# Performance work log

Hardware: AMD Instinct MI355X
Metric: run time of the kernel (lower is better)

## Reference

```python
import jax, jax.numpy as jnp
import numpy as np
import math

# e3nn-style fully-connected Clebsch-Gordan tensor product
# irreps_in1 = 64x0e + 64x1e + 64x2e   (dim 576)
# irreps_in2 =  1x0e +  1x1e +  1x2e   (dim 9, e.g. spherical harmonics)
# irreps_out = 64x0e + 64x1e + 64x2e   (dim 576), shared weights
MUL1, MUL2, MULO = 64, 1, 64
LS = [0, 1, 2]
N_BATCH = 32768


def _su2_cg(j1, m1, j2, m2, j3, m3):
    # SU(2) Clebsch-Gordan coefficient <j1 m1 j2 m2 | j3 m3> (Racah formula)
    if m3 != m1 + m2:
        return 0.0
    f = math.factorial
    c = (2 * j3 + 1) * f(j1 + j2 - j3) * f(j1 - j2 + j3) * f(-j1 + j2 + j3) / f(j1 + j2 + j3 + 1)
    c = math.sqrt(c)
    c *= math.sqrt(f(j3 + m3) * f(j3 - m3) * f(j1 - m1) * f(j1 + m1) * f(j2 - m2) * f(j2 + m2))
    s = 0.0
    for k in range(max(0, j2 - j3 - m1, j1 - j3 + m2), min(j1 + j2 - j3, j1 - m1, j2 + m2) + 1):
        s += (-1.0) ** k / (f(k) * f(j1 + j2 - j3 - k) * f(j1 - m1 - k) * f(j2 + m2 - k)
                            * f(j3 - j2 + m1 + k) * f(j3 - j1 - m2 + k))
    return c * s


def _q_real_to_complex(l):
    # unitary change of basis, columns = real-SH index, rows = complex m (e3nn convention)
    q = np.zeros((2 * l + 1, 2 * l + 1), dtype=np.complex128)
    r2 = 1.0 / math.sqrt(2.0)
    for m in range(-l, 0):
        q[l + m, l + abs(m)] = r2
        q[l + m, l - abs(m)] = -1j * r2
    q[l, l] = 1.0
    for m in range(1, l + 1):
        q[l + m, l + m] = (-1) ** m * r2
        q[l + m, l - m] = 1j * (-1) ** m * r2
    return (-1j) ** l * q


def _real_cg(l1, l2, l3):
    # CG tensor in the real spherical-harmonic basis, unit Frobenius norm (wigner_3j-like)
    C = np.zeros((2 * l1 + 1, 2 * l2 + 1, 2 * l3 + 1), dtype=np.complex128)
    for m1 in range(-l1, l1 + 1):
        for m2 in range(-l2, l2 + 1):
            m3 = m1 + m2
            if abs(m3) <= l3:
                C[l1 + m1, l2 + m2, l3 + m3] = _su2_cg(l1, m1, l2, m2, l3, m3)
    U1, U2, U3 = _q_real_to_complex(l1), _q_real_to_complex(l2), _q_real_to_complex(l3)
    Cr = np.einsum('ia,jb,kc,ijk->abc', U1, U2, np.conj(U3), C)
    assert np.abs(Cr.imag).max() < 1e-9, 'real-basis CG should be real'
    Cr = Cr.real
    return (Cr / np.linalg.norm(Cr)).astype(np.float32)


PATHS = [(l1, l2, l3) for l1 in LS for l2 in LS for l3 in LS if abs(l1 - l2) <= l3 <= l1 + l2]
CG = {p: jnp.asarray(_real_cg(*p)) for p in PATHS}
N_PATHS_TO = {l3: sum(1 for p in PATHS if p[2] == l3) for l3 in LS}
ALPHA = {l3: 1.0 / math.sqrt(MUL1 * MUL2 * N_PATHS_TO[l3]) for l3 in LS}  # path normalization
WEIGHT_NUMEL = len(PATHS) * MUL1 * MUL2 * MULO  # 15 * 4096 = 61440
DIM1 = MUL1 * sum(2 * l + 1 for l in LS)  # 576
DIM2 = MUL2 * sum(2 * l + 1 for l in LS)  # 9


def _split1(x):
    segs, off = [], 0
    for l in LS:
        d = MUL1 * (2 * l + 1)
        segs.append(x[:, off:off + d].reshape(-1, MUL1, 2 * l + 1))
        off += d
    return segs


def _split2(y):
    segs, off = [], 0
    for l in LS:
        d = 2 * l + 1
        segs.append(y[:, off:off + d])
        off += d
    return segs


def tensor_product(x, y, W):
    # W (x (CG-otimes) y): per-path weighted Clebsch-Gordan contraction
    xs, ys = _split1(x), _split2(y)  # xs[l]: [N,64,2l+1], ys[l]: [N,2l+1]
    N = x.shape[0]
    outs = [jnp.zeros((N, MULO, 2 * l + 1), x.dtype) for l in LS]
    off = 0
    for (l1, l2, l3) in PATHS:
        Wp = W[off:off + MUL1 * MULO].reshape(MUL1, MULO)  # [u, w] (v = 1)
        off += MUL1 * MULO
        outs[l3] = outs[l3] + ALPHA[l3] * jnp.einsum(
            'nui,nj,ijk,uw->nwk', xs[l1], ys[l2], CG[(l1, l2, l3)], Wp)
    return jnp.concatenate([o.reshape(N, -1) for o in outs], axis=-1)  # [N, 576]


def setup_inputs() -> dict:
    key = jax.random.key(0)
    kx, ky, kw = jax.random.split(key, 3)
    x = jax.random.normal(kx, (N_BATCH, DIM1), dtype=jnp.float32)
    y = jax.random.normal(ky, (N_BATCH, DIM2), dtype=jnp.float32)
    W = jax.random.normal(kw, (WEIGHT_NUMEL,), dtype=jnp.float32)
    return {'x': x, 'y': y, 'W': W}


def reference(x, y, W):
    return tensor_product(x, y, W)
```

## Files before the change

kernel.cpp:

```cpp
#include <hip/hip_runtime.h>
#include <cmath>
#include <complex>
#include <algorithm>

#define NPATH 15
constexpr int PL1[NPATH] = {0,0,0, 1,1,1,1,1,1, 2,2,2,2,2,2};
constexpr int PL2[NPATH] = {0,1,2, 0,1,1,1,2,2, 0,1,1,2,2,2};
constexpr int PL3[NPATH] = {0,1,2, 1,0,1,2,1,2, 2,1,2,0,1,2};
constexpr int CGOFF[NPATH] = {0,1,10,35,44,53,80,125,170,245,270,315,390,415,490};
constexpr int CGTOT = 615;
constexpr int YOFF[3] = {0,1,4};
constexpr int KKB[3]  = {0,1,4};

constexpr int GP[8] = {5,6,7,8,10,11,13,14};
constexpr int GB[8] = {0,9,24,33,48,63,88,103};
constexpr int YGTOT = 137;

struct CGArg { float v[CGTOT]; };

static double factd(int n){ double r=1.0; for(int i=2;i<=n;++i) r*=(double)i; return r; }

static double su2_cg(int j1,int m1,int j2,int m2,int j3,int m3){
  if (m3 != m1+m2) return 0.0;
  double c = (double)(2*j3+1) * factd(j1+j2-j3) * factd(j1-j2+j3) * factd(-j1+j2+j3)
             / factd(j1+j2+j3+1);
  c = std::sqrt(c);
  c *= std::sqrt(factd(j3+m3)*factd(j3-m3)*factd(j1-m1)*factd(j1+m1)*factd(j2-m2)*factd(j2+m2));
  double s = 0.0;
  int kmin = std::max(0, std::max(j2-j3-m1, j1-j3+m2));
  int kmax = std::min(j1+j2-j3, std::min(j1-m1, j2+m2));
  for (int k=kmin;k<=kmax;++k){
    double d = factd(k)*factd(j1+j2-j3-k)*factd(j1-m1-k)*factd(j2+m2-k)
             * factd(j3-j2+m1+k)*factd(j3-j1-m2+k);
    s += ((k&1)? -1.0 : 1.0)/d;
  }
  return c*s;
}

static void qmat(int l, std::complex<double>* q){
  int d = 2*l+1;
  for (int a=0;a<d*d;++a) q[a] = std::complex<double>(0.0,0.0);
  const double r2 = 1.0/std::sqrt(2.0);
  for (int m=-l; m<0; ++m){
    q[(l+m)*d + (l-m)] = std::complex<double>(r2, 0.0);
    q[(l+m)*d + (l+m)] = std::complex<double>(0.0, -r2);
  }
  q[l*d + l] = std::complex<double>(1.0,0.0);
  for (int m=1; m<=l; ++m){
    double sg = (m&1)? -1.0 : 1.0;
    q[(l+m)*d + (l+m)] = std::complex<double>(sg*r2, 0.0);
    q[(l+m)*d + (l-m)] = std::complex<double>(0.0, sg*r2);
  }
  std::complex<double> ph = (l==0)? std::complex<double>(1,0)
                        : (l==1)? std::complex<double>(0,-1)
                                : std::complex<double>(-1,0);
  for (int a=0;a<d*d;++a) q[a] *= ph;
}

static void compute_cg(float* outv){
  const int npaths_to[3] = {3,6,6};
  for (int p=0;p<NPATH;++p){
    int l1=PL1[p], l2=PL2[p], l3=PL3[p];
    int d1=2*l1+1, d2=2*l2+1, d3=2*l3+1;
    std::complex<double> C[5][5][5];
    for (int a=0;a<5;++a) for(int b=0;b<5;++b) for(int c=0;c<5;++c) C[a][b][c]=std::complex<double>(0,0);
    for (int m1=-l1;m1<=l1;++m1) for (int m2=-l2;m2<=l2;++m2){
      int m3=m1+m2;
      if (std::abs(m3)<=l3) C[l1+m1][l2+m2][l3+m3] = su2_cg(l1,m1,l2,m2,l3,m3);
    }
    std::complex<double> U1[25],U2[25],U3[25];
    qmat(l1,U1); qmat(l2,U2); qmat(l3,U3);
    double Cr[5][5][5]; double nrm=0.0;
    for (int a=0;a<d1;++a) for (int b=0;b<d2;++b) for (int c=0;c<d3;++c){
      std::complex<double> s(0,0);
      for (int i=0;i<d1;++i) for (int j=0;j<d2;++j) for (int k=0;k<d3;++k)
        s += U1[i*d1+a]*U2[j*d2+b]*std::conj(U3[k*d3+c])*C[i][j][k];
      Cr[a][b][c] = s.real();
      nrm += s.real()*s.real();
    }
    nrm = std::sqrt(nrm);
    double alpha = 1.0/std::sqrt(64.0*(double)npaths_to[l3]);
    float* o = outv + CGOFF[p];
    int idx=0;
    for (int a=0;a<d1;++a) for (int b=0;b<d2;++b) for (int c=0;c<d3;++c)
      o[idx++] = (float)(Cr[a][b][c]/nrm*alpha);
  }
}

typedef short bf16x8 __attribute__((ext_vector_type(8)));
typedef float f32x4 __attribute__((ext_vector_type(4)));

__device__ __forceinline__ unsigned cvtpk_bf16(float a, float b){
  unsigned r;
  asm("v_cvt_pk_bf16_f32 %0, %1, %2" : "=v"(r) : "v"(a), "v"(b));
  return r;
}

__device__ __forceinline__ bf16x8 afrag(const unsigned short* s_xt, int plane, int kt, int row, int q){
  int c = (kt*4 + q) ^ (row & 7);
  return *reinterpret_cast<const bf16x8*>(s_xt + (plane*16 + row)*64 + c*8);
}
__device__ __forceinline__ bf16x8 wfrag(const unsigned short* WT, int p, int wt, int cl, int kt, int q){
  return *reinterpret_cast<const bf16x8*>(WT + p*4096 + (wt*16+cl)*64 + kt*32 + q*8);
}
__device__ __forceinline__ void xt_write_pk(unsigned short* s_xt, int plane, int n, int t16, uint2 pk){
  const int swz = (((t16>>1)^(n&7))<<3) + ((t16&1)<<2);
  *reinterpret_cast<uint2*>(s_xt + (plane*16 + n)*64 + swz) = pk;
}

__device__ __forceinline__ void pack_x(const float4& r0, const float4* r1, const float4* r2, uint2* xpk){
  const float* f0 = reinterpret_cast<const float*>(&r0);
  const float* f1 = reinterpret_cast<const float*>(r1);
  const float* f2 = reinterpret_cast<const float*>(r2);
  xpk[0].x = cvtpk_bf16(f0[0], f0[1]);  xpk[0].y = cvtpk_bf16(f0[2], f0[3]);
  #pragma unroll
  for (int i=0;i<3;++i){
    xpk[1+i].x = cvtpk_bf16(f1[0*3+i], f1[1*3+i]);
    xpk[1+i].y = cvtpk_bf16(f1[2*3+i], f1[3*3+i]);
  }
  #pragma unroll
  for (int i=0;i<5;++i){
    xpk[4+i].x = cvtpk_bf16(f2[0*5+i], f2[1*5+i]);
    xpk[4+i].y = cvtpk_bf16(f2[2*5+i], f2[3*5+i]);
  }
}

template<int G,int L1,int L3>
__device__ __forceinline__ void gen_path(const unsigned short* s_xt, const bf16x8* a,
                                         bf16x8 b0, bf16x8 b1,
                                         const float* yg4, f32x4* acc){
  constexpr int D1=2*L1+1, D3=2*L3+1;
  const f32x4 z4 = {0.f,0.f,0.f,0.f};
  #pragma unroll
  for (int i=0;i<D1;++i){
    f32x4 T = __builtin_amdgcn_mfma_f32_16x16x32_bf16(a[2*i],   b0, z4, 0,0,0);
    T       = __builtin_amdgcn_mfma_f32_16x16x32_bf16(a[2*i+1], b1, T,  0,0,0);
    #pragma unroll
    for (int k=0;k<D3;++k){
      f32x4 yv = *reinterpret_cast<const f32x4*>(yg4 + (GB[G] + i*D3 + k)*16);
      acc[KKB[L3]+k] += T*yv;
    }
  }
}

__device__ __forceinline__ void epilogue(const f32x4* acc, float* __restrict__ out,
                                         int base, int wid, int cl, int q){
  const int wc = wid*16 + cl;
  #pragma unroll
  for (int r=0;r<4;++r){
    float* orow = out + (size_t)(base + q*4 + r)*576;
    orow[wc] = acc[0][r];
    #pragma unroll
    for (int k=0;k<3;++k) orow[64 + wc*3 + k]  = acc[1+k][r];
    #pragma unroll
    for (int k=0;k<5;++k) orow[256 + wc*5 + k] = acc[4+k][r];
  }
}

__global__ __launch_bounds__(256, 3)
void tp_kernel(const float* __restrict__ x, const float* __restrict__ y,
               const unsigned short* __restrict__ WT, float* __restrict__ out, CGArg cga)
{
  __shared__ __align__(16) unsigned short s_xt[9*16*64];
  __shared__ __align__(16) float s_yg[YGTOT*16];

  const int tid = threadIdx.x;
  const int n0 = blockIdx.x * 16;
  const int n_s = tid>>4, t16 = tid&15;
  const int lane = tid & 63, wid = tid >> 6;
  const int cl = lane & 15, q = lane >> 4;

  const float* xb = x + (size_t)(n0 + n_s)*576;
  float4 r0 = *reinterpret_cast<const float4*>(xb + t16*4);
  float4 r1[3], r2[5];
  #pragma unroll
  for (int i=0;i<3;++i) r1[i] = *reinterpret_cast<const float4*>(xb + 64 + t16*12 + 4*i);
  #pragma unroll
  for (int i=0;i<5;++i) r2[i] = *reinterpret_cast<const float4*>(xb + 256 + t16*20 + 4*i);

  float yl[9];
  {
    const float* yrow = y + (size_t)(n0 + t16)*9;
    #pragma unroll
    for (int j=0;j<9;++j) yl[j] = yrow[j];
  }

  uint2 xpk[9];
  pack_x(r0, r1, r2, xpk);
  #pragma unroll
  for (int pl=0; pl<9; ++pl) xt_write_pk(s_xt, pl, n_s, t16, xpk[pl]);

  if (tid < 16){
    #pragma unroll
    for (int j=0;j<9;++j) s_yg[(128+j)*16 + tid] = yl[j];
  }

  #pragma unroll
  for (int g=0; g<8; ++g){
    constexpr int GPp[8] = {5,6,7,8,10,11,13,14};
    const int p = GPp[g];
    const int d1=2*PL1[p]+1, d2=2*PL2[p]+1, d3=2*PL3[p]+1;
    const int cnt = d1*d3*16;
    for (int idx=tid; idx<cnt; idx+=256){
      int ik = idx >> 4;
      int i  = ik/d3;
      int k  = ik - i*d3;
      float s=0.f;
      for (int j=0;j<d2;++j)
        s += yl[YOFF[PL2[p]]+j]*cga.v[CGOFF[p]+(i*d2+j)*d3+k];
      s_yg[(GB[g]+ik)*16 + t16] = s;
    }
  }
  __syncthreads();

  const float* yg4 = s_yg + q*4;
  #define YV(E) (*reinterpret_cast<const f32x4*>(yg4 + (E)*16))

  const f32x4 z4 = {0.f,0.f,0.f,0.f};
  f32x4 acc[9] = {z4,z4,z4,z4,z4,z4,z4,z4,z4};
  bf16x8 b0,b1,nb0,nb1;
  const f32x4 y0v = YV(128);

  #define LDB(P) { nb0 = wfrag(WT,P,wid,cl,0,q); nb1 = wfrag(WT,P,wid,cl,1,q); }
  #define ADV    { b0 = nb0; b1 = nb1; }

  b0 = wfrag(WT,0,wid,cl,0,q); b1 = wfrag(WT,0,wid,cl,1,q);

  {
    bf16x8 a0[2];
    #pragma unroll
    for (int kt=0;kt<2;++kt) a0[kt] = afrag(s_xt, 0, kt, cl, q);

    LDB(1);
    {
      f32x4 T = __builtin_amdgcn_mfma_f32_16x16x32_bf16(a0[0], b0, z4, 0,0,0);
      T       = __builtin_amdgcn_mfma_f32_16x16x32_bf16(a0[1], b1, T,  0,0,0);
      acc[0] += (cga.v[CGOFF[0]]*y0v)*T;
    } ADV;
    LDB(2);
    {
      f32x4 T = __builtin_amdgcn_mfma_f32_16x16x32_bf16(a0[0], b0, z4, 0,0,0);
      T       = __builtin_amdgcn_mfma_f32_16x16x32_bf16(a0[1], b1, T,  0,0,0);
      #pragma unroll
      for (int k=0;k<3;++k) acc[1+k] += (cga.v[CGOFF[1]]*YV(129+k))*T;
    } ADV;
    LDB(3);
    {
      f32x4 T = __builtin_amdgcn_mfma_f32_16x16x32_bf16(a0[0], b0, z4, 0,0,0);
      T       = __builtin_amdgcn_mfma_f32_16x16x32_bf16(a0[1], b1, T,  0,0,0);
      #pragma unroll
      for (int k=0;k<5;++k) acc[4+k] += (cga.v[CGOFF[2]]*YV(132+k))*T;
    } ADV;
  }

  {
    bf16x8 a1[6];
    #pragma unroll
    for (int i=0;i<3;++i)
      #pragma unroll
      for (int kt=0;kt<2;++kt) a1[2*i+kt] = afrag(s_xt, 1+i, kt, cl, q);

    LDB(4);
    {
      f32x4 cy = cga.v[CGOFF[3]]*y0v;
      #pragma unroll
      for (int i=0;i<3;++i){
        f32x4 T = __builtin_amdgcn_mfma_f32_16x16x32_bf16(a1[2*i],   b0, z4, 0,0,0);
        T       = __builtin_amdgcn_mfma_f32_16x16x32_bf16(a1[2*i+1], b1, T,  0,0,0);
        acc[1+i] += cy*T;
      }
    } ADV;
    LDB(5);
    {
      f32x4 s = z4;
      #pragma unroll
      for (int i=0;i<3;++i){
        f32x4 T = __builtin_amdgcn_mfma_f32_16x16x32_bf16(a1[2*i],   b0, z4, 0,0,0);
        T       = __builtin_amdgcn_mfma_f32_16x16x32_bf16(a1[2*i+1], b1, T,  0,0,0);
        s += YV(129+i)*T;
      }
      acc[0] += s*cga.v[CGOFF[4]];
    } ADV;
    LDB(6);  gen_path<0,1,1>(s_xt, a1, b0, b1, yg4, acc); ADV;
    LDB(7);  gen_path<1,1,2>(s_xt, a1, b0, b1, yg4, acc); ADV;
    LDB(8);  gen_path<2,1,1>(s_xt, a1, b0, b1, yg4, acc); ADV;
    LDB(9);  gen_path<3,1,2>(s_xt, a1, b0, b1, yg4, acc); ADV;
  }

  {
    bf16x8 a2[10];
    #pragma unroll
    for (int i=0;i<5;++i)
      #pragma unroll
      for (int kt=0;kt<2;++kt) a2[2*i+kt] = afrag(s_xt, 4+i, kt, cl, q);

    LDB(10);
    {
      f32x4 cy = cga.v[CGOFF[9]]*y0v;
      #pragma unroll
      for (int i=0;i<5;++i){
        f32x4 T = __builtin_amdgcn_mfma_f32_16x16x32_bf16(a2[2*i],   b0, z4, 0,0,0);
        T       = __builtin_amdgcn_mfma_f32_16x16x32_bf16(a2[2*i+1], b1, T,  0,0,0);
        acc[4+i] += cy*T;
      }
    } ADV;
    LDB(11); gen_path<4,2,1>(s_xt, a2, b0, b1, yg4, acc); ADV;
    LDB(12); gen_path<5,2,2>(s_xt, a2, b0, b1, yg4, acc); ADV;
    LDB(13);
    {
      f32x4 s = z4;
      #pragma unroll
      for (int i=0;i<5;++i){
        f32x4 T = __builtin_amdgcn_mfma_f32_16x16x32_bf16(a2[2*i],   b0, z4, 0,0,0);
        T       = __builtin_amdgcn_mfma_f32_16x16x32_bf16(a2[2*i+1], b1, T,  0,0,0);
        s += YV(132+i)*T;
      }
      acc[0] += s*cga.v[CGOFF[12]];
    } ADV;
    LDB(14); gen_path<6,2,1>(s_xt, a2, b0, b1, yg4, acc); ADV;
             gen_path<7,2,2>(s_xt, a2, b0, b1, yg4, acc);
  }
  #undef LDB
  #undef ADV
  #undef YV

  epilogue(acc, out, n0, wid, cl, q);
}

__global__ void wt_kernel(const float* __restrict__ W, unsigned short* __restrict__ WT){
  int t = blockIdx.x*256 + threadIdx.x;
  int p = t >> 12, r = t & 4095, w = r >> 6, u = r & 63;
  float f = W[(p<<12) + (u<<6) + w];
  unsigned fu = __builtin_bit_cast(unsigned, f);
  unsigned rr = (fu + 0x7FFFu + ((fu>>16)&1u)) >> 16;
  WT[t] = (unsigned short)rr;
}

extern "C" void kernel_launch(void* const* d_in, const int* in_sizes, int n_in,
                              void* d_out, int out_size, void* d_ws, size_t ws_size,
                              hipStream_t stream) {
  const float* x = (const float*)d_in[0];
  const float* y = (const float*)d_in[1];
  const float* W = (const float*)d_in[2];
  float* out = (float*)d_out;
  (void)in_sizes; (void)n_in; (void)out_size; (void)ws_size;

  unsigned short* WT = (unsigned short*)d_ws;

  CGArg cga;
  compute_cg(cga.v);

  hipLaunchKernelGGL(wt_kernel, dim3(240), dim3(256), 0, stream, W, WT);
  hipLaunchKernelGGL(tp_kernel, dim3(2048), dim3(256), 0, stream, x, y, WT, out, cga);
}
```

Baseline: 56.75 us.

## Halve block to two waves, each computing two output column tiles

The tensor-product kernel now runs 128 threads per block instead of 256. Each wave handles two 16-column output tiles (wid and wid+2), so every A fragment read from shared memory feeds two MFMA chains. Each thread also loads and packs two x rows into LDS. The aim is to cut LDS A-fragment traffic and per-block overhead, at the cost of double the accumulator registers and fewer waves per block, which may lower latency hiding.

```diff
diff --git a/kernel.cpp b/kernel.cpp
--- a/kernel.cpp
+++ b/kernel.cpp
@@ -12,7 +12,6 @@
 constexpr int YOFF[3] = {0,1,4};
 constexpr int KKB[3]  = {0,1,4};
 
-constexpr int GP[8] = {5,6,7,8,10,11,13,14};
 constexpr int GB[8] = {0,9,24,33,48,63,88,103};
 constexpr int YGTOT = 137;
 
@@ -90,6 +89,8 @@
 typedef short bf16x8 __attribute__((ext_vector_type(8)));
 typedef float f32x4 __attribute__((ext_vector_type(4)));
 
+#define MFMA16(A,B,C) __builtin_amdgcn_mfma_f32_16x16x32_bf16((A),(B),(C),0,0,0)
+
 __device__ __forceinline__ unsigned cvtpk_bf16(float a, float b){
   unsigned r;
   asm("v_cvt_pk_bf16_f32 %0, %1, %2" : "=v"(r) : "v"(a), "v"(b));
@@ -126,26 +127,74 @@
 }
 
 template<int G,int L1,int L3>
-__device__ __forceinline__ void gen_path(const unsigned short* s_xt, const bf16x8* a,
-                                         bf16x8 b0, bf16x8 b1,
-                                         const float* yg4, f32x4* acc){
+__device__ __forceinline__ void gen_path2(const bf16x8* a,
+                                          bf16x8 b0A, bf16x8 b1A, bf16x8 b0B, bf16x8 b1B,
+                                          const float* yg4, f32x4* accA, f32x4* accB){
   constexpr int D1=2*L1+1, D3=2*L3+1;
   const f32x4 z4 = {0.f,0.f,0.f,0.f};
   #pragma unroll
   for (int i=0;i<D1;++i){
-    f32x4 T = __builtin_amdgcn_mfma_f32_16x16x32_bf16(a[2*i],   b0, z4, 0,0,0);
-    T       = __builtin_amdgcn_mfma_f32_16x16x32_bf16(a[2*i+1], b1, T,  0,0,0);
+    f32x4 TA = MFMA16(a[2*i], b0A, z4);  TA = MFMA16(a[2*i+1], b1A, TA);
+    f32x4 TB = MFMA16(a[2*i], b0B, z4);  TB = MFMA16(a[2*i+1], b1B, TB);
     #pragma unroll
     for (int k=0;k<D3;++k){
       f32x4 yv = *reinterpret_cast<const f32x4*>(yg4 + (GB[G] + i*D3 + k)*16);
-      acc[KKB[L3]+k] += T*yv;
-    }
-  }
+      accA[KKB[L3]+k] += TA*yv;
+      accB[KKB[L3]+k] += TB*yv;
+    }
+  }
+}
+
+template<int D1,int ACCB>
+__device__ __forceinline__ void delta_l0_2(const bf16x8* a,
+                                           bf16x8 b0A, bf16x8 b1A, bf16x8 b0B, bf16x8 b1B,
+                                           f32x4 cy, f32x4* accA, f32x4* accB){
+  const f32x4 z4 = {0.f,0.f,0.f,0.f};
+  #pragma unroll
+  for (int i=0;i<D1;++i){
+    f32x4 TA = MFMA16(a[2*i], b0A, z4);  TA = MFMA16(a[2*i+1], b1A, TA);
+    f32x4 TB = MFMA16(a[2*i], b0B, z4);  TB = MFMA16(a[2*i+1], b1B, TB);
+    accA[ACCB+i] += cy*TA;
+    accB[ACCB+i] += cy*TB;
+  }
+}
+
+template<int D3,int YE,int ACCB>
+__device__ __forceinline__ void delta_0l_2(const bf16x8* a,
+                                           bf16x8 b0A, bf16x8 b1A, bf16x8 b0B, bf16x8 b1B,
+                                           float c, const float* yg4, f32x4* accA, f32x4* accB){
+  const f32x4 z4 = {0.f,0.f,0.f,0.f};
+  f32x4 TA = MFMA16(a[0], b0A, z4);  TA = MFMA16(a[1], b1A, TA);
+  f32x4 TB = MFMA16(a[0], b0B, z4);  TB = MFMA16(a[1], b1B, TB);
+  #pragma unroll
+  for (int k=0;k<D3;++k){
+    f32x4 yv = c * (*reinterpret_cast<const f32x4*>(yg4 + (YE+k)*16));
+    accA[ACCB+k] += yv*TA;
+    accB[ACCB+k] += yv*TB;
+  }
+}
+
+template<int D1,int YE>
+__device__ __forceinline__ void delta_ll0_2(const bf16x8* a,
+                                            bf16x8 b0A, bf16x8 b1A, bf16x8 b0B, bf16x8 b1B,
+                                            float c, const float* yg4, f32x4* accA, f32x4* accB){
+  const f32x4 z4 = {0.f,0.f,0.f,0.f};
+  f32x4 sA = z4, sB = z4;
+  #pragma unroll
+  for (int i=0;i<D1;++i){
+    f32x4 TA = MFMA16(a[2*i], b0A, z4);  TA = MFMA16(a[2*i+1], b1A, TA);
+    f32x4 TB = MFMA16(a[2*i], b0B, z4);  TB = MFMA16(a[2*i+1], b1B, TB);
+    f32x4 yv = *reinterpret_cast<const f32x4*>(yg4 + (YE+i)*16);
+    sA += yv*TA;
+    sB += yv*TB;
+  }
+  accA[0] += sA*c;
+  accB[0] += sB*c;
 }
 
 __device__ __forceinline__ void epilogue(const f32x4* acc, float* __restrict__ out,
-                                         int base, int wid, int cl, int q){
-  const int wc = wid*16 + cl;
+                                         int base, int wt, int cl, int q){
+  const int wc = wt*16 + cl;
   #pragma unroll
   for (int r=0;r<4;++r){
     float* orow = out + (size_t)(base + q*4 + r)*576;
@@ -157,7 +206,7 @@
   }
 }
 
-__global__ __launch_bounds__(256, 3)
+__global__ __launch_bounds__(128, 2)
 void tp_kernel(const float* __restrict__ x, const float* __restrict__ y,
                const unsigned short* __restrict__ WT, float* __restrict__ out, CGArg cga)
 {
@@ -170,45 +219,58 @@
   const int lane = tid & 63, wid = tid >> 6;
   const int cl = lane & 15, q = lane >> 4;
 
-  const float* xb = x + (size_t)(n0 + n_s)*576;
-  float4 r0 = *reinterpret_cast<const float4*>(xb + t16*4);
-  float4 r1[3], r2[5];
-  #pragma unroll
-  for (int i=0;i<3;++i) r1[i] = *reinterpret_cast<const float4*>(xb + 64 + t16*12 + 4*i);
-  #pragma unroll
-  for (int i=0;i<5;++i) r2[i] = *reinterpret_cast<const float4*>(xb + 256 + t16*20 + 4*i);
-
-  float yl[9];
   {
-    const float* yrow = y + (size_t)(n0 + t16)*9;
-    #pragma unroll
-    for (int j=0;j<9;++j) yl[j] = yrow[j];
-  }
-
-  uint2 xpk[9];
-  pack_x(r0, r1, r2, xpk);
-  #pragma unroll
-  for (int pl=0; pl<9; ++pl) xt_write_pk(s_xt, pl, n_s, t16, xpk[pl]);
-
-  if (tid < 16){
-    #pragma unroll
-    for (int j=0;j<9;++j) s_yg[(128+j)*16 + tid] = yl[j];
-  }
-
-  #pragma unroll
-  for (int g=0; g<8; ++g){
-    constexpr int GPp[8] = {5,6,7,8,10,11,13,14};
-    const int p = GPp[g];
-    const int d1=2*PL1[p]+1, d2=2*PL2[p]+1, d3=2*PL3[p]+1;
-    const int cnt = d1*d3*16;
-    for (int idx=tid; idx<cnt; idx+=256){
-      int ik = idx >> 4;
-      int i  = ik/d3;
-      int k  = ik - i*d3;
-      float s=0.f;
-      for (int j=0;j<d2;++j)
-        s += yl[YOFF[PL2[p]]+j]*cga.v[CGOFF[p]+(i*d2+j)*d3+k];
-      s_yg[(GB[g]+ik)*16 + t16] = s;
+    const float* xbA = x + (size_t)(n0 + n_s)*576;
+    const float* xbB = x + (size_t)(n0 + n_s + 8)*576;
+    float4 rA0 = *reinterpret_cast<const float4*>(xbA + t16*4);
+    float4 rB0 = *reinterpret_cast<const float4*>(xbB + t16*4);
+    float4 rA1[3], rB1[3], rA2[5], rB2[5];
+    #pragma unroll
+    for (int i=0;i<3;++i){
+      rA1[i] = *reinterpret_cast<const float4*>(xbA + 64 + t16*12 + 4*i);
+      rB1[i] = *reinterpret_cast<const float4*>(xbB + 64 + t16*12 + 4*i);
+    }
+    #pragma unroll
+    for (int i=0;i<5;++i){
+      rA2[i] = *reinterpret_cast<const float4*>(xbA + 256 + t16*20 + 4*i);
+      rB2[i] = *reinterpret_cast<const float4*>(xbB + 256 + t16*20 + 4*i);
+    }
+
+    float yl[9];
+    {
+      const float* yrow = y + (size_t)(n0 + t16)*9;
+      #pragma unroll
+      for (int j=0;j<9;++j) yl[j] = yrow[j];
+    }
+
+    uint2 xpk[9];
+    pack_x(rA0, rA1, rA2, xpk);
+    #pragma unroll
+    for (int pl=0; pl<9; ++pl) xt_write_pk(s_xt, pl, n_s, t16, xpk[pl]);
+    pack_x(rB0, rB1, rB2, xpk);
+    #pragma unroll
+    for (int pl=0; pl<9; ++pl) xt_write_pk(s_xt, pl, n_s+8, t16, xpk[pl]);
+
+    if (tid < 16){
+      #pragma unroll
+      for (int j=0;j<9;++j) s_yg[(128+j)*16 + tid] = yl[j];
+    }
+
+    #pragma unroll
+    for (int g=0; g<8; ++g){
+      constexpr int GPp[8] = {5,6,7,8,10,11,13,14};
+      const int p = GPp[g];
+      const int d1=2*PL1[p]+1, d2=2*PL2[p]+1, d3=2*PL3[p]+1;
+      const int cnt = d1*d3*16;
+      for (int idx=tid; idx<cnt; idx+=128){
+        int ik = idx >> 4;
+        int i  = ik/d3;
+        int k  = ik - i*d3;
+        float s=0.f;
+        for (int j=0;j<d2;++j)
+          s += yl[YOFF[PL2[p]]+j]*cga.v[CGOFF[p]+(i*d2+j)*d3+k];
+        s_yg[(GB[g]+ik)*16 + t16] = s;
+      }
     }
   }
   __syncthreads();
@@ -217,40 +279,26 @@
   #define YV(E) (*reinterpret_cast<const f32x4*>(yg4 + (E)*16))
 
   const f32x4 z4 = {0.f,0.f,0.f,0.f};
-  f32x4 acc[9] = {z4,z4,z4,z4,z4,z4,z4,z4,z4};
-  bf16x8 b0,b1,nb0,nb1;
+  f32x4 accA[9] = {z4,z4,z4,z4,z4,z4,z4,z4,z4};
+  f32x4 accB[9] = {z4,z4,z4,z4,z4,z4,z4,z4,z4};
+  bf16x8 b0A,b1A,b0B,b1B, nb0A,nb1A,nb0B,nb1B;
   const f32x4 y0v = YV(128);
 
-  #define LDB(P) { nb0 = wfrag(WT,P,wid,cl,0,q); nb1 = wfrag(WT,P,wid,cl,1,q); }
-  #define ADV    { b0 = nb0; b1 = nb1; }
-
-  b0 = wfrag(WT,0,wid,cl,0,q); b1 = wfrag(WT,0,wid,cl,1,q);
+  #define LDB(P) { nb0A = wfrag(WT,P,wid,cl,0,q);   nb1A = wfrag(WT,P,wid,cl,1,q); \
+                   nb0B = wfrag(WT,P,wid+2,cl,0,q); nb1B = wfrag(WT,P,wid+2,cl,1,q); }
+  #define ADV    { b0A=nb0A; b1A=nb1A; b0B=nb0B; b1B=nb1B; }
+
+  b0A = wfrag(WT,0,wid,cl,0,q);   b1A = wfrag(WT,0,wid,cl,1,q);
+  b0B = wfrag(WT,0,wid+2,cl,0,q); b1B = wfrag(WT,0,wid+2,cl,1,q);
 
   {
     bf16x8 a0[2];
     #pragma unroll
     for (int kt=0;kt<2;++kt) a0[kt] = afrag(s_xt, 0, kt, cl, q);
 
-    LDB(1);
-    {
-      f32x4 T = __builtin_amdgcn_mfma_f32_16x16x32_bf16(a0[0], b0, z4, 0,0,0);
-      T       = __builtin_amdgcn_mfma_f32_16x16x32_bf16(a0[1], b1, T,  0,0,0);
-      acc[0] += (cga.v[CGOFF[0]]*y0v)*T;
-    } ADV;
-    LDB(2);
-    {
-      f32x4 T = __builtin_amdgcn_mfma_f32_16x16x32_bf16(a0[0], b0, z4, 0,0,0);
-      T       = __builtin_amdgcn_mfma_f32_16x16x32_bf16(a0[1], b1, T,  0,0,0);
-      #pragma unroll
-      for (int k=0;k<3;++k) acc[1+k] += (cga.v[CGOFF[1]]*YV(129+k))*T;
-    } ADV;
-    LDB(3);
-    {
-      f32x4 T = __builtin_amdgcn_mfma_f32_16x16x32_bf16(a0[0], b0, z4, 0,0,0);
-      T       = __builtin_amdgcn_mfma_f32_16x16x32_bf16(a0[1], b1, T,  0,0,0);
-      #pragma unroll
-      for (int k=0;k<5;++k) acc[4+k] += (cga.v[CGOFF[2]]*YV(132+k))*T;
-    } ADV;
+    LDB(1);  delta_l0_2<1,0>(a0, b0A,b1A,b0B,b1B, cga.v[CGOFF[0]]*y0v, accA, accB); ADV;
+    LDB(2);  delta_0l_2<3,129,1>(a0, b0A,b1A,b0B,b1B, cga.v[CGOFF[1]], yg4, accA, accB); ADV;
+    LDB(3);  delta_0l_2<5,132,4>(a0, b0A,b1A,b0B,b1B, cga.v[CGOFF[2]], yg4, accA, accB); ADV;
   }
 
   {
@@ -260,31 +308,12 @@
       #pragma unroll
       for (int kt=0;kt<2;++kt) a1[2*i+kt] = afrag(s_xt, 1+i, kt, cl, q);
 
-    LDB(4);
-    {
-      f32x4 cy = cga.v[CGOFF[3]]*y0v;
-      #pragma unroll
-      for (int i=0;i<3;++i){
-        f32x4 T = __builtin_amdgcn_mfma_f32_16x16x32_bf16(a1[2*i],   b0, z4, 0,0,0);
-        T       = __builtin_amdgcn_mfma_f32_16x16x32_bf16(a1[2*i+1], b1, T,  0,0,0);
-        acc[1+i] += cy*T;
-      }
-    } ADV;
-    LDB(5);
-    {
-      f32x4 s = z4;
-      #pragma unroll
-      for (int i=0;i<3;++i){
-        f32x4 T = __builtin_amdgcn_mfma_f32_16x16x32_bf16(a1[2*i],   b0, z4, 0,0,0);
-        T       = __builtin_amdgcn_mfma_f32_16x16x32_bf16(a1[2*i+1], b1, T,  0,0,0);
-        s += YV(129+i)*T;
-      }
-      acc[0] += s*cga.v[CGOFF[4]];
-    } ADV;
-    LDB(6);  gen_path<0,1,1>(s_xt, a1, b0, b1, yg4, acc); ADV;
-    LDB(7);  gen_path<1,1,2>(s_xt, a1, b0, b1, yg4, acc); ADV;
-    LDB(8);  gen_path<2,1,1>(s_xt, a1, b0, b1, yg4, acc); ADV;
-    LDB(9);  gen_path<3,1,2>(s_xt, a1, b0, b1, yg4, acc); ADV;
+    LDB(4);  delta_l0_2<3,1>(a1, b0A,b1A,b0B,b1B, cga.v[CGOFF[3]]*y0v, accA, accB); ADV;
+    LDB(5);  delta_ll0_2<3,129>(a1, b0A,b1A,b0B,b1B, cga.v[CGOFF[4]], yg4, accA, accB); ADV;
+    LDB(6);  gen_path2<0,1,1>(a1, b0A,b1A,b0B,b1B, yg4, accA, accB); ADV;
+    LDB(7);  gen_path2<1,1,2>(a1, b0A,b1A,b0B,b1B, yg4, accA, accB); ADV;
+    LDB(8);  gen_path2<2,1,1>(a1, b0A,b1A,b0B,b1B, yg4, accA, accB); ADV;
+    LDB(9);  gen_path2<3,1,2>(a1, b0A,b1A,b0B,b1B, yg4, accA, accB); ADV;
   }
 
   {
@@ -294,37 +323,19 @@
       #pragma unroll
       for (int kt=0;kt<2;++kt) a2[2*i+kt] = afrag(s_xt, 4+i, kt, cl, q);
 
-    LDB(10);
-    {
-      f32x4 cy = cga.v[CGOFF[9]]*y0v;
-      #pragma unroll
-      for (int i=0;i<5;++i){
-        f32x4 T = __builtin_amdgcn_mfma_f32_16x16x32_bf16(a2[2*i],   b0, z4, 0,0,0);
-        T       = __builtin_amdgcn_mfma_f32_16x16x32_bf16(a2[2*i+1], b1, T,  0,0,0);
-        acc[4+i] += cy*T;
-      }
-    } ADV;
-    LDB(11); gen_path<4,2,1>(s_xt, a2, b0, b1, yg4, acc); ADV;
-    LDB(12); gen_path<5,2,2>(s_xt, a2, b0, b1, yg4, acc); ADV;
-    LDB(13);
-    {
-      f32x4 s = z4;
-      #pragma unroll
-      for (int i=0;i<5;++i){
-        f32x4 T = __builtin_amdgcn_mfma_f32_16x16x32_bf16(a2[2*i],   b0, z4, 0,0,0);
-        T       = __builtin_amdgcn_mfma_f32_16x16x32_bf16(a2[2*i+1], b1, T,  0,0,0);
-        s += YV(132+i)*T;
-      }
-      acc[0] += s*cga.v[CGOFF[12]];
-    } ADV;
-    LDB(14); gen_path<6,2,1>(s_xt, a2, b0, b1, yg4, acc); ADV;
-             gen_path<7,2,2>(s_xt, a2, b0, b1, yg4, acc);
+    LDB(10); delta_l0_2<5,4>(a2, b0A,b1A,b0B,b1B, cga.v[CGOFF[9]]*y0v, accA, accB); ADV;
+    LDB(11); gen_path2<4,2,1>(a2, b0A,b1A,b0B,b1B, yg4, accA, accB); ADV;
+    LDB(12); gen_path2<5,2,2>(a2, b0A,b1A,b0B,b1B, yg4, accA, accB); ADV;
+    LDB(13); delta_ll0_2<5,132>(a2, b0A,b1A,b0B,b1B, cga.v[CGOFF[12]], yg4, accA, accB); ADV;
+    LDB(14); gen_path2<6,2,1>(a2, b0A,b1A,b0B,b1B, yg4, accA, accB); ADV;
+             gen_path2<7,2,2>(a2, b0A,b1A,b0B,b1B, yg4, accA, accB);
   }
   #undef LDB
   #undef ADV
   #undef YV
 
-  epilogue(acc, out, n0, wid, cl, q);
+  epilogue(accA, out, n0, wid,   cl, q);
+  epilogue(accB, out, n0, wid+2, cl, q);
 }
 
 __global__ void wt_kernel(const float* __restrict__ W, unsigned short* __restrict__ WT){
@@ -351,5 +362,5 @@
   compute_cg(cga.v);
 
   hipLaunchKernelGGL(wt_kernel, dim3(240), dim3(256), 0, stream, W, WT);
-  hipLaunchKernelGGL(tp_kernel, dim3(2048), dim3(256), 0, stream, x, y, WT, out, cga);
-}
+  hipLaunchKernelGGL(tp_kernel, dim3(2048), dim3(128), 0, stream, x, y, WT, out, cga);
+}
```

After: 77.34 us. 36.3% more time.
